# Performance work log

Hardware: AMD Instinct MI355X
Metric: run time of the kernel (lower is better)

## Reference

```python
import jax, jax.numpy as jnp
import numpy as np

L, B, Q, P, D, H, F = 3, 256, 128, 16, 256, 16, 512
DK = D // H
SCALE = DK ** -0.5  # lsa=False -> constant scale
EPS = 1e-5


def _ln(x, g, b):
    m = jnp.mean(x, axis=-1, keepdims=True)
    v = jnp.mean(jnp.square(x - m), axis=-1, keepdims=True)
    return (x - m) * jax.lax.rsqrt(v + EPS) * g + b


def setup_inputs() -> dict:
    key = jax.random.key(0)
    ks = jax.random.split(key, 12)
    w = lambda k, shape: 0.02 * jax.random.normal(k, shape, dtype=jnp.float32)
    return {
        "x": jax.random.normal(ks[0], (B, Q, P), dtype=jnp.float32),
        "attn_bias": 0.1 * jax.random.normal(ks[1], (1, Q, Q), dtype=jnp.float32),
        "W_P": w(ks[2], (P, D)), "b_P": jnp.zeros((D,), jnp.float32),
        "W_pos": w(ks[3], (Q, D)),
        "Wq": w(ks[4], (L, D, D)), "bq": jnp.zeros((L, D), jnp.float32),
        "Wk": w(ks[5], (L, D, D)), "bk": jnp.zeros((L, D), jnp.float32),
        "Wv": w(ks[6], (L, D, D)), "bv": jnp.zeros((L, D), jnp.float32),
        "Wo": w(ks[7], (L, D, D)), "bo": jnp.zeros((L, D), jnp.float32),
        "ln1_g": jnp.ones((L, D), jnp.float32), "ln1_b": jnp.zeros((L, D), jnp.float32),
        "W1": w(ks[8], (L, D, F)), "b1": jnp.zeros((L, F), jnp.float32),
        "W2": w(ks[9], (L, F, D)), "b2": jnp.zeros((L, D), jnp.float32),
        "ln2_g": jnp.ones((L, D), jnp.float32), "ln2_b": jnp.zeros((L, D), jnp.float32),
    }


def _encoder(x, attn_bias, W_P, b_P, W_pos,
             Wq, bq, Wk, bk, Wv, bv, Wo, bo, ln1_g, ln1_b,
             W1, b1, W2, b2, ln2_g, ln2_b):
    # patch embedding + positional encoding (dropout=0, eval mode)
    z = x @ W_P + b_P + W_pos                      # [B, Q, D]
    bias = attn_bias[:, None]                      # [1, 1, Q, Q]

    def layer(carry, p):
        z, prev = carry
        (wq, bq_, wk, bk_, wv, bv_, wo, bo_, g1, be1, w1, b1_, w2, b2_, g2, be2) = p
        q = (z @ wq + bq_).reshape(B, Q, H, DK).transpose(0, 2, 1, 3)  # [B,H,Q,dk]
        k = (z @ wk + bk_).reshape(B, Q, H, DK).transpose(0, 2, 1, 3)
        v = (z @ wv + bv_).reshape(B, Q, H, DK).transpose(0, 2, 1, 3)
        # residual-attention + bias-augmented scores
        scores = jnp.einsum('bhqd,bhkd->bhqk', q, k) * SCALE + prev + bias
        attn = jax.nn.softmax(scores, axis=-1)
        o = jnp.einsum('bhqk,bhkd->bhqd', attn, v)
        o = o.transpose(0, 2, 1, 3).reshape(B, Q, D) @ wo + bo_
        z = _ln(z + o, g1, be1)                     # post-norm
        ffo = jax.nn.gelu(z @ w1 + b1_, approximate=False) @ w2 + b2_
        z = _ln(z + ffo, g2, be2)
        return (z, scores), None

    prev0 = jnp.zeros((B, H, Q, Q), z.dtype)        # prev=None == add zero
    params = (Wq, bq, Wk, bk, Wv, bv, Wo, bo, ln1_g, ln1_b,
              W1, b1, W2, b2, ln2_g, ln2_b)
    (z, _), _ = jax.lax.scan(layer, (z, prev0), params)
    return z


def reference(x, attn_bias, W_P, b_P, W_pos, Wq, bq, Wk, bk, Wv, bv, Wo, bo,
              ln1_g, ln1_b, W1, b1, W2, b2, ln2_g, ln2_b):
    return _encoder(x, attn_bias, W_P, b_P, W_pos, Wq, bq, Wk, bk, Wv, bv,
                    Wo, bo, ln1_g, ln1_b, W1, b1, W2, b2, ln2_g, ln2_b)
```

## Files before the change

### kernel.cpp

```cpp
#include <hip/hip_runtime.h>

#define DEV __device__ __forceinline__

typedef float          f32x4  __attribute__((ext_vector_type(4)));
typedef __bf16         bf16x8 __attribute__((ext_vector_type(8)));
typedef unsigned short u16x8  __attribute__((ext_vector_type(8)));

static constexpr int  Bq   = 256;
static constexpr int  Qs   = 128;
static constexpr int  Dm   = 256;
static constexpr int  Ff   = 512;
static constexpr int  ROWS = Bq * Qs;
static constexpr long QK_LSTR = (long)ROWS * 512;

DEV float b2f(unsigned short h) {
    unsigned int u = ((unsigned int)h) << 16;
    float f; __builtin_memcpy(&f, &u, 4); return f;
}
DEV unsigned short f2b(float f) {
    unsigned int u; __builtin_memcpy(&u, &f, 4);
    u += 0x7fffu + ((u >> 16) & 1u);
    return (unsigned short)(u >> 16);
}
DEV f32x4 mfma_bf16(u16x8 a, u16x8 b, f32x4 c) {
    return __builtin_amdgcn_mfma_f32_16x16x32_bf16(
        __builtin_bit_cast(bf16x8, a), __builtin_bit_cast(bf16x8, b), c, 0, 0, 0);
}
DEV void gl_lds16(const unsigned short* g, unsigned short* l) {
    __builtin_amdgcn_global_load_lds(
        (const __attribute__((address_space(1))) unsigned int*)g,
        (__attribute__((address_space(3))) unsigned int*)l, 16, 0, 0);
}
DEV int zadr(int row, int col) {
    return row * 256 + ((((col >> 3) ^ (row & 7))) << 3) + (col & 7);
}

__global__ void k_embed(const float* __restrict__ x,
                        const float* __restrict__ WP,
                        const float* __restrict__ bP,
                        const float* __restrict__ Wpos,
                        unsigned short* __restrict__ zb) {
    int row = blockIdx.x;
    int d   = threadIdx.x;
    int q   = row & (Qs - 1);
    const float* xr = x + row * 16;
    float acc = bP[d] + Wpos[q * Dm + d];
#pragma unroll
    for (int p = 0; p < 16; p++) acc += xr[p] * WP[p * Dm + d];
    zb[(long)row * Dm + d] = f2b(acc);
}

static constexpr int S0 = 3 * 768 * 256;
static constexpr int S1 = 3 * 256 * 256;
static constexpr int S2 = 3 * 512 * 256;
static constexpr int S3 = 3 * 256 * 512;
static constexpr int S4 = 3 * 768;
static constexpr int S5 = 3 * 64 * 256;
static constexpr int PREP_TOT = S0 + S1 + S2 + S3 + S4 + S5;

__global__ void k_prep(const float* __restrict__ Wq, const float* __restrict__ Wk,
                       const float* __restrict__ Wv, const float* __restrict__ Wo,
                       const float* __restrict__ W1, const float* __restrict__ W2,
                       const float* __restrict__ bq, const float* __restrict__ bk,
                       const float* __restrict__ bv, const float* __restrict__ ab,
                       unsigned short* __restrict__ wTqkv, unsigned short* __restrict__ wTo,
                       unsigned short* __restrict__ wp1, unsigned short* __restrict__ wp2,
                       float* __restrict__ bqkv, float* __restrict__ pb) {
    int idx = blockIdx.x * 256 + threadIdx.x;
    if (idx < S0) {
        int l = idx / (768 * 256), r = idx % (768 * 256);
        int n = r / 256, k = r % 256;
        const float* W = (n < 256) ? Wq : (n < 512) ? Wk : Wv;
        float v = W[(long)l * 65536 + k * 256 + (n & 255)];
        if (n < 256) v *= 0.25f;
        wTqkv[idx] = f2b(v);
    } else if (idx < S0 + S1) {
        int j = idx - S0;
        int l = j / 65536, r = j % 65536, n = r / 256, k = r % 256;
        wTo[j] = f2b(Wo[(long)l * 65536 + k * 256 + n]);
    } else if (idx < S0 + S1 + S2) {
        int j = idx - S0 - S1;
        int l = j / 131072, r = j % 131072;
        int tile = r >> 9, le = r & 511, lane = le >> 3, e = le & 7;
        int ntile = tile >> 3, kk = tile & 7;
        int n = ntile * 16 + (lane & 15), k = kk * 32 + (lane >> 4) * 8 + e;
        wp1[j] = f2b(W1[(long)l * 131072 + k * 512 + n]);
    } else if (idx < S0 + S1 + S2 + S3) {
        int j = idx - S0 - S1 - S2;
        int l = j / 131072, r = j % 131072;
        int tile = r >> 9, le = r & 511, lane = le >> 3, e = le & 7;
        int ntile = tile >> 4, kk = tile & 15;
        int n = ntile * 16 + (lane & 15), k = kk * 32 + (lane >> 4) * 8 + e;
        wp2[j] = f2b(W2[(long)l * 131072 + k * 256 + n]);
    } else if (idx < S0 + S1 + S2 + S3 + S4) {
        int j = idx - S0 - S1 - S2 - S3;
        int l = j / 768, c = j % 768;
        float v = (c < 256) ? bq[l * 256 + c] * 0.25f
                : (c < 512) ? bk[l * 256 + c - 256]
                            : bv[l * 256 + c - 512];
        bqkv[j] = v;
    } else if (idx < PREP_TOT) {
        int j = idx - S0 - S1 - S2 - S3 - S4;
        int l = j / 16384, r = j % 16384;
        int u = r / 256, t = r % 256;
        int i = u >> 5, rr = (u >> 3) & 3, jj = u & 7;
        int wave = t >> 6, quad = (t >> 4) & 3, l16 = t & 15;
        int m = 32 * wave + 16 * i + 4 * quad + rr;
        int col = 16 * jj + l16;
        pb[j] = (float)(l + 1) * ab[m * 128 + col];
    }
}

template <int GELU, int MODE>
__global__ __launch_bounds__(256) void k_gemm(const unsigned short* __restrict__ A,
                                              const unsigned short* __restrict__ WT,
                                              const float* __restrict__ bias,
                                              unsigned short* __restrict__ outB,
                                              unsigned short* __restrict__ aux,
                                              int M, int N, int K) {
    __shared__ unsigned short smem[16384];
    unsigned short* As = smem;
    unsigned short* Bs = smem + 8192;
    const int tid  = threadIdx.x;
    const int wave = tid >> 6, lane = tid & 63, quad = lane >> 4, l16 = lane & 15;
    const int mq = wave >> 1, nq = wave & 1;
    const int m_blk = blockIdx.x * 128, n_blk = blockIdx.y * 128;
    const int c0 = tid, c1 = tid + 256;
    const int ra0 = c0 >> 2, ca0 = (c0 & 3) * 8;
    const int ra1 = c1 >> 2, ca1 = (c1 & 3) * 8;

    f32x4 acc[4][4] = {};

    for (int k0 = 0; k0 < K; k0 += 64) {
#pragma unroll
        for (int hh = 0; hh < 2; hh++) {
            int kk = k0 + hh * 32;
            gl_lds16(A  + (long)(m_blk + ra0) * K + kk + ca0, &As[hh * 4096 + c0 * 8]);
            gl_lds16(A  + (long)(m_blk + ra1) * K + kk + ca1, &As[hh * 4096 + c1 * 8]);
            gl_lds16(WT + (long)(n_blk + ra0) * K + kk + ca0, &Bs[hh * 4096 + c0 * 8]);
            gl_lds16(WT + (long)(n_blk + ra1) * K + kk + ca1, &Bs[hh * 4096 + c1 * 8]);
        }
        __syncthreads();
#pragma unroll
        for (int hh = 0; hh < 2; hh++) {
            u16x8 af[4], bf[4];
#pragma unroll
            for (int i = 0; i < 4; i++)
                af[i] = *(const u16x8*)&As[hh * 4096 + (64 * mq + 16 * i + l16) * 32 + quad * 8];
#pragma unroll
            for (int j = 0; j < 4; j++)
                bf[j] = *(const u16x8*)&Bs[hh * 4096 + (64 * nq + 16 * j + l16) * 32 + quad * 8];
#pragma unroll
            for (int i = 0; i < 4; i++)
#pragma unroll
                for (int j = 0; j < 4; j++)
                    acc[i][j] = mfma_bf16(af[i], bf[j], acc[i][j]);
        }
        __syncthreads();
    }

#pragma unroll
    for (int i = 0; i < 4; i++) {
        int rl = 64 * mq + 16 * i + quad * 4;
#pragma unroll
        for (int j = 0; j < 4; j++) {
            int cl = 64 * nq + 16 * j + l16;
            float bb = bias[n_blk + cl];
#pragma unroll
            for (int r = 0; r < 4; r++) {
                float v = acc[i][j][r] + bb;
                if (GELU) v = 0.5f * v * (1.0f + erff(v * 0.70710678118f));
                if (MODE == 0) smem[(rl + r) * 128 + cl] = f2b(v);
                if (MODE == 2) {
                    int g = 4 * nq + j;
                    smem[g * 2048 + (rl + r) * 16 + l16] = f2b(v);
                }
            }
        }
    }
    __syncthreads();
#pragma unroll
    for (int c = tid; c < 2048; c += 256) {
        u16x8 val = *(const u16x8*)&smem[c * 8];
        if (MODE == 0) {
            int row = c >> 4, seg = c & 15;
            *(u16x8*)&outB[(long)(m_blk + row) * N + n_blk + seg * 8] = val;
        }
        if (MODE == 2) {
            int g = c >> 8, w = c & 255;
            int n = n_blk + g * 16;
            if (n < 512) {
                int s = n >> 8, h = (n >> 4) & 15;
                *(u16x8*)&outB[((long)(((m_blk >> 7) * 16 + h) * 2 + s)) * 2048 + w * 8] = val;
            } else {
                int hh = (n - 512) >> 4;
                *(u16x8*)&aux[((long)hh * ROWS + m_blk) * 16 + w * 8] = val;
            }
        }
    }
}

template <int LAST, int AHM>
__global__ __launch_bounds__(256) void k_gemm_ln(const unsigned short* __restrict__ A,
                                                 const unsigned short* __restrict__ WT,
                                                 const float* __restrict__ bias,
                                                 const unsigned short* __restrict__ Zres,
                                                 const float* __restrict__ g,
                                                 const float* __restrict__ be,
                                                 unsigned short* __restrict__ zb,
                                                 float* __restrict__ outF,
                                                 int K) {
    __shared__ unsigned short smem[16384 + 2048 + 8192];
    unsigned short* Zs = smem;
    unsigned short* As = smem + 16384;
    unsigned short* Bs = smem + 16384 + 2048;
    float2* stats = (float2*)(smem + 16384);

    const int tid  = threadIdx.x;
    const int wave = tid >> 6, lane = tid & 63, quad = lane >> 4, l16 = lane & 15;
    const int m_blk = blockIdx.x * 64;

#pragma unroll
    for (int s = 0; s < 8; s++) {
        int c = tid + 256 * s;
        int zr = c >> 5, zc = (c & 31) * 8;
        gl_lds16(Zres + (long)(m_blk + zr) * 256 + zc, &Zs[c * 8]);
    }

    const int ca = (tid & 3) * 8, raA = tid >> 2;
    f32x4 acc[4][4] = {};

    for (int k0 = 0; k0 < K; k0 += 32) {
        if (AHM) {
            int k = k0 + ca;
            gl_lds16(A + ((long)(k >> 4) * ROWS + m_blk + raA) * 16 + (k & 15), &As[tid * 8]);
        } else {
            gl_lds16(A + (long)(m_blk + raA) * K + k0 + ca, &As[tid * 8]);
        }
#pragma unroll
        for (int s = 0; s < 4; s++) {
            int c = tid + 256 * s;
            int br = c >> 2, bc = (c & 3) * 8;
            gl_lds16(WT + (long)br * K + k0 + bc, &Bs[c * 8]);
        }
        __syncthreads();
        u16x8 af[4], bf[4];
#pragma unroll
        for (int i = 0; i < 4; i++)
            af[i] = *(const u16x8*)&As[(16 * i + l16) * 32 + quad * 8];
#pragma unroll
        for (int j = 0; j < 4; j++)
            bf[j] = *(const u16x8*)&Bs[(64 * wave + 16 * j + l16) * 32 + quad * 8];
#pragma unroll
        for (int i = 0; i < 4; i++)
#pragma unroll
            for (int j = 0; j < 4; j++)
                acc[i][j] = mfma_bf16(af[i], bf[j], acc[i][j]);
        __syncthreads();
    }

    float bb[4], gg[4], bt[4];
#pragma unroll
    for (int j = 0; j < 4; j++) {
        int col = 64 * wave + 16 * j + l16;
        bb[j] = bias[col]; gg[j] = g[col]; bt[j] = be[col];
    }
#pragma unroll
    for (int i = 0; i < 4; i++) {
#pragma unroll
        for (int r = 0; r < 4; r++) {
            int rloc = 16 * i + quad * 4 + r;
            float s1 = 0.f, s2 = 0.f;
#pragma unroll
            for (int j = 0; j < 4; j++) {
                int col = 64 * wave + 16 * j + l16;
                float v = acc[i][j][r] + bb[j] + b2f(Zs[rloc * 256 + col]);
                acc[i][j][r] = v;
                s1 += v; s2 += v * v;
            }
            for (int mk = 1; mk < 16; mk <<= 1) {
                s1 += __shfl_xor(s1, mk);
                s2 += __shfl_xor(s2, mk);
            }
            if (l16 == 0) stats[rloc * 4 + wave] = make_float2(s1, s2);
        }
    }
    __syncthreads();
#pragma unroll
    for (int i = 0; i < 4; i++) {
#pragma unroll
        for (int r = 0; r < 4; r++) {
            int rloc = 16 * i + quad * 4 + r;
            f32x4 p0 = *(const f32x4*)&stats[rloc * 4];
            f32x4 p1 = *(const f32x4*)&stats[rloc * 4 + 2];
            float S1 = p0[0] + p0[2] + p1[0] + p1[2];
            float S2 = p0[1] + p0[3] + p1[1] + p1[3];
            float mean = S1 * (1.0f / 256.0f);
            float var  = S2 * (1.0f / 256.0f) - mean * mean;
            float rstd = rsqrtf(var + 1e-5f);
            long grow = m_blk + rloc;
#pragma unroll
            for (int j = 0; j < 4; j++) {
                int col = 64 * wave + 16 * j + l16;
                float o = (acc[i][j][r] - mean) * rstd * gg[j] + bt[j];
                if (LAST) outF[grow * 256 + col] = o;
                else      zb[grow * 256 + col] = f2b(o);
            }
        }
    }
}

template <int LAST>
__global__ __launch_bounds__(256, 2) void k_ffn(const unsigned short* __restrict__ zin,
                                                const unsigned short* __restrict__ wp1,
                                                const float* __restrict__ b1,
                                                const unsigned short* __restrict__ wp2,
                                                const float* __restrict__ b2,
                                                const float* __restrict__ g2,
                                                const float* __restrict__ be2,
                                                unsigned short* __restrict__ zout,
                                                float* __restrict__ outF) {
    __shared__ unsigned short Zs[64 * 256];
    __shared__ unsigned short Hs[64 * 256];
    __shared__ float2 stats[64 * 4];

    const int tid  = threadIdx.x;
    const int wave = tid >> 6, lane = tid & 63, quad = (lane >> 4) & 3, l16 = lane & 15;
    const int m_blk = blockIdx.x * 64;

    {
        int row = tid >> 2;
#pragma unroll
        for (int cc = 0; cc < 8; cc++) {
            int c0 = (tid & 3) * 64 + cc * 8;
            u16x8 v = *(const u16x8*)&zin[(long)(m_blk + row) * 256 + c0];
            *(u16x8*)&Zs[zadr(row, c0)] = v;
        }
    }
    __syncthreads();

    f32x4 z2[4][4] = {};
#pragma unroll 1
    for (int c = 0; c < 2; c++) {
        f32x4 a1[4][4] = {};
#pragma unroll 2
        for (int kk = 0; kk < 8; kk++) {
            u16x8 af[4], bf[4];
#pragma unroll
            for (int i = 0; i < 4; i++)
                af[i] = *(const u16x8*)&Zs[(16 * i + l16) * 256 + (((kk * 4 + quad) ^ (l16 & 7)) << 3)];
#pragma unroll
            for (int j = 0; j < 4; j++)
                bf[j] = *(const u16x8*)&wp1[((long)(16 * c + 4 * wave + j) * 8 + kk) * 512 + lane * 8];
#pragma unroll
            for (int i = 0; i < 4; i++)
#pragma unroll
                for (int j = 0; j < 4; j++)
                    a1[i][j] = mfma_bf16(af[i], bf[j], a1[i][j]);
        }
        __syncthreads();
        float b1v[4];
#pragma unroll
        for (int j = 0; j < 4; j++) b1v[j] = b1[256 * c + 64 * wave + 16 * j + l16];
#pragma unroll
        for (int i = 0; i < 4; i++)
#pragma unroll
            for (int j = 0; j < 4; j++)
#pragma unroll
                for (int r = 0; r < 4; r++) {
                    int row  = 16 * i + quad * 4 + r;
                    int colh = 64 * wave + 16 * j + l16;
                    float v = a1[i][j][r] + b1v[j];
                    float gel = 0.5f * v * (1.0f + erff(v * 0.70710678118f));
                    Hs[zadr(row, colh)] = f2b(gel);
                }
        __syncthreads();
#pragma unroll 2
        for (int kk = 0; kk < 8; kk++) {
            u16x8 af[4], bf[4];
#pragma unroll
            for (int i = 0; i < 4; i++)
                af[i] = *(const u16x8*)&Hs[(16 * i + l16) * 256 + (((kk * 4 + quad) ^ (l16 & 7)) << 3)];
#pragma unroll
            for (int j = 0; j < 4; j++)
                bf[j] = *(const u16x8*)&wp2[((long)(4 * wave + j) * 16 + 8 * c + kk) * 512 + lane * 8];
#pragma unroll
            for (int i = 0; i < 4; i++)
#pragma unroll
                for (int j = 0; j < 4; j++)
                    z2[i][j] = mfma_bf16(af[i], bf[j], z2[i][j]);
        }
    }

    float b2v[4], gg[4], bb[4];
#pragma unroll
    for (int j = 0; j < 4; j++) {
        int col = 64 * wave + 16 * j + l16;
        b2v[j] = b2[col]; gg[j] = g2[col]; bb[j] = be2[col];
    }
#pragma unroll
    for (int i = 0; i < 4; i++)
#pragma unroll
        for (int r = 0; r < 4; r++) {
            int row = 16 * i + quad * 4 + r;
            float s1 = 0.f, s2 = 0.f;
#pragma unroll
            for (int j = 0; j < 4; j++) {
                int col = 64 * wave + 16 * j + l16;
                float v = z2[i][j][r] + b2v[j] + b2f(Zs[zadr(row, col)]);
                z2[i][j][r] = v; s1 += v; s2 += v * v;
            }
            for (int mk = 1; mk < 16; mk <<= 1) { s1 += __shfl_xor(s1, mk); s2 += __shfl_xor(s2, mk); }
            if (l16 == 0) stats[row * 4 + wave] = make_float2(s1, s2);
        }
    __syncthreads();
#pragma unroll
    for (int i = 0; i < 4; i++)
#pragma unroll
        for (int r = 0; r < 4; r++) {
            int row = 16 * i + quad * 4 + r;
            f32x4 p0 = *(const f32x4*)&stats[row * 4];
            f32x4 p1 = *(const f32x4*)&stats[row * 4 + 2];
            float S1 = p0[0] + p0[2] + p1[0] + p1[2];
            float S2 = p0[1] + p0[3] + p1[1] + p1[3];
            float mean = S1 * (1.0f / 256.0f);
            float var  = S2 * (1.0f / 256.0f) - mean * mean;
            float rstd = rsqrtf(var + 1e-5f);
            long grow = m_blk + row;
#pragma unroll
            for (int j = 0; j < 4; j++) {
                int col = 64 * wave + 16 * j + l16;
                float o = (z2[i][j][r] - mean) * rstd * gg[j] + bb[j];
                if (LAST) outF[grow * 256 + col] = o;
                else      zout[grow * 256 + col] = f2b(o);
            }
        }
}

template <int L>
__global__ __launch_bounds__(256) void k_attn(const unsigned short* __restrict__ qkh,
                                              const unsigned short* __restrict__ vbuf,
                                              const float* __restrict__ pb,
                                              unsigned short* __restrict__ o_out) {
    __shared__ unsigned short vt[16 * 136];
    __shared__ unsigned short Ps[128 * 136];
    const int tid  = threadIdx.x;
    const int wave = tid >> 6, lane = tid & 63, quad = lane >> 4, l16 = lane & 15;
    const int b = blockIdx.x >> 4, h = blockIdx.x & 15;
    const int qrow = tid >> 1, half = tid & 1;

    u16x8 vv = *(const u16x8*)(vbuf + ((long)h * ROWS + b * Qs + qrow) * 16 + half * 8);
    const float* pbt = pb + (long)L * 16384 + tid;

    f32x4 accS[2][8] = {};
    u16x8 zero = {};

    constexpr int FULL = (L + 1) / 2;
    constexpr bool HALF = ((L + 1) & 1) != 0;

#pragma unroll
    for (int p = 0; p < FULL; p++) {
        const unsigned short* q0 = qkh + ((long)(((2 * p) * Bq + b) * 16 + h) * 2) * 2048;
        const unsigned short* q1 = qkh + ((long)(((2 * p + 1) * Bq + b) * 16 + h) * 2) * 2048;
        const unsigned short* qsel = (quad < 2) ? q0 : q1;
        const unsigned short* ksel = (quad < 2) ? (q0 + 2048) : (q1 + 2048);
        const int koff = (quad & 1) * 8;
        u16x8 af[2], bf8[8];
#pragma unroll
        for (int i = 0; i < 2; i++) {
            int m = 32 * wave + 16 * i + l16;
            af[i] = *(const u16x8*)(qsel + m * 16 + koff);
        }
#pragma unroll
        for (int j = 0; j < 8; j++) {
            int n = 16 * j + l16;
            bf8[j] = *(const u16x8*)(ksel + n * 16 + koff);
        }
#pragma unroll
        for (int i = 0; i < 2; i++)
#pragma unroll
            for (int j = 0; j < 8; j++)
                accS[i][j] = mfma_bf16(af[i], bf8[j], accS[i][j]);
    }
    if (HALF) {
        const unsigned short* qt = qkh + ((long)((L * Bq + b) * 16 + h) * 2) * 2048;
        const unsigned short* kt = qt + 2048;
        u16x8 af[2], bf8[8];
#pragma unroll
        for (int i = 0; i < 2; i++) {
            int m = 32 * wave + 16 * i + l16;
            af[i] = (quad < 2) ? *(const u16x8*)(qt + m * 16 + quad * 8) : zero;
        }
#pragma unroll
        for (int j = 0; j < 8; j++) {
            int n = 16 * j + l16;
            bf8[j] = (quad < 2) ? *(const u16x8*)(kt + n * 16 + quad * 8) : zero;
        }
#pragma unroll
        for (int i = 0; i < 2; i++)
#pragma unroll
            for (int j = 0; j < 8; j++)
                accS[i][j] = mfma_bf16(af[i], bf8[j], accS[i][j]);
    }

#pragma unroll
    for (int jj = 0; jj < 8; jj++) vt[(half * 8 + jj) * 136 + qrow] = vv[jj];

#pragma unroll
    for (int i = 0; i < 2; i++) {
#pragma unroll
        for (int r = 0; r < 4; r++) {
            int m = 32 * wave + 16 * i + quad * 4 + r;
#pragma unroll
            for (int j = 0; j < 8; j++) {
                int u = (i * 4 + r) * 8 + j;
                float s = accS[i][j][r] + pbt[u * 256];
                Ps[m * 136 + 16 * j + l16] = f2b(__expf(s));
            }
        }
    }
    __syncthreads();

    f32x4 accO[2] = {};
    f32x4 accR[2] = {};
    u16x8 ones;
#pragma unroll
    for (int jj = 0; jj < 8; jj++) ones[jj] = 0x3F80;
#pragma unroll
    for (int s = 0; s < 4; s++) {
        u16x8 bv = *(const u16x8*)&vt[l16 * 136 + s * 32 + quad * 8];
#pragma unroll
        for (int i = 0; i < 2; i++) {
            u16x8 ap = *(const u16x8*)&Ps[(32 * wave + 16 * i + l16) * 136 + s * 32 + quad * 8];
            accO[i] = mfma_bf16(ap, bv, accO[i]);
            accR[i] = mfma_bf16(ap, ones, accR[i]);
        }
    }
    __syncthreads();
#pragma unroll
    for (int i = 0; i < 2; i++)
#pragma unroll
        for (int r = 0; r < 4; r++) {
            int m = 32 * wave + 16 * i + quad * 4 + r;
            float inv = __builtin_amdgcn_rcpf(accR[i][r]);
            vt[m * 16 + l16] = f2b(accO[i][r] * inv);
        }
    __syncthreads();
    {
        unsigned short* obase = o_out + ((long)h * ROWS + b * Qs) * 16;
        *(u16x8*)&obase[tid * 8] = *(const u16x8*)&vt[tid * 8];
    }
}

extern "C" void kernel_launch(void* const* d_in, const int* in_sizes, int n_in,
                              void* d_out, int out_size, void* d_ws, size_t ws_size,
                              hipStream_t stream) {
    const float* x     = (const float*)d_in[0];
    const float* abias = (const float*)d_in[1];
    const float* WP    = (const float*)d_in[2];
    const float* bP    = (const float*)d_in[3];
    const float* Wpos  = (const float*)d_in[4];
    const float* Wq    = (const float*)d_in[5];
    const float* bqp   = (const float*)d_in[6];
    const float* Wk    = (const float*)d_in[7];
    const float* bkp   = (const float*)d_in[8];
    const float* Wv    = (const float*)d_in[9];
    const float* bvp   = (const float*)d_in[10];
    const float* Wo    = (const float*)d_in[11];
    const float* bo    = (const float*)d_in[12];
    const float* g1    = (const float*)d_in[13];
    const float* be1   = (const float*)d_in[14];
    const float* W1    = (const float*)d_in[15];
    const float* b1    = (const float*)d_in[16];
    const float* W2    = (const float*)d_in[17];
    const float* b2    = (const float*)d_in[18];
    const float* g2    = (const float*)d_in[19];
    const float* be2   = (const float*)d_in[20];
    (void)in_sizes; (void)n_in; (void)out_size; (void)ws_size;

    char* ws = (char*)d_ws;
    size_t off = 0;
    auto alloc = [&](size_t bytes) -> char* {
        char* p = ws + off; off += (bytes + 255) & ~(size_t)255; return p;
    };
    unsigned short* z_b   = (unsigned short*)alloc((size_t)ROWS * Dm * 2);
    unsigned short* qkh   = (unsigned short*)alloc((size_t)3 * ROWS * 512 * 2);
    unsigned short* v_cur = (unsigned short*)alloc((size_t)ROWS * Dm * 2);
    unsigned short* o_b   = (unsigned short*)alloc((size_t)ROWS * Dm * 2);
    unsigned short* wTqkv = (unsigned short*)alloc((size_t)S0 * 2);
    unsigned short* wTo   = (unsigned short*)alloc((size_t)S1 * 2);
    unsigned short* wp1   = (unsigned short*)alloc((size_t)S2 * 2);
    unsigned short* wp2   = (unsigned short*)alloc((size_t)S3 * 2);
    float*          bqkv  = (float*)alloc((size_t)S4 * 4);
    float*          pb    = (float*)alloc((size_t)S5 * 4);

    k_prep<<<(PREP_TOT + 255) / 256, 256, 0, stream>>>(
        Wq, Wk, Wv, Wo, W1, W2, bqp, bkp, bvp, abias,
        wTqkv, wTo, wp1, wp2, bqkv, pb);
    k_embed<<<ROWS, 256, 0, stream>>>(x, WP, bP, Wpos, z_b);

    for (int l = 0; l < 3; l++) {
        k_gemm<0, 2><<<dim3(ROWS / 128, 6), 256, 0, stream>>>(
            z_b, wTqkv + (long)l * 768 * 256, bqkv + l * 768,
            qkh + (long)l * QK_LSTR, v_cur, ROWS, 768, 256);
        if (l == 0)      k_attn<0><<<Bq * 16, 256, 0, stream>>>(qkh, v_cur, pb, o_b);
        else if (l == 1) k_attn<1><<<Bq * 16, 256, 0, stream>>>(qkh, v_cur, pb, o_b);
        else             k_attn<2><<<Bq * 16, 256, 0, stream>>>(qkh, v_cur, pb, o_b);
        k_gemm_ln<0, 1><<<ROWS / 64, 256, 0, stream>>>(
            o_b, wTo + (long)l * 256 * 256, bo + l * 256, z_b,
            g1 + l * 256, be1 + l * 256, z_b, nullptr, 256);
        if (l == 2)
            k_ffn<1><<<ROWS / 64, 256, 0, stream>>>(
                z_b, wp1 + (long)l * 131072, b1 + l * 512,
                wp2 + (long)l * 131072, b2 + l * 256,
                g2 + l * 256, be2 + l * 256, nullptr, (float*)d_out);
        else
            k_ffn<0><<<ROWS / 64, 256, 0, stream>>>(
                z_b, wp1 + (long)l * 131072, b1 + l * 512,
                wp2 + (long)l * 131072, b2 + l * 256,
                g2 + l * 256, be2 + l * 256, z_b, nullptr);
    }
}
```

Before: 500.3 us.

## Fuse output projection and first LayerNorm into the FFN kernel

Removes the separate k_gemm_ln launch by computing the attention output projection, residual add and LayerNorm inside k_ffn, keeping the normalized rows in LDS for the FFN instead of writing z to global memory and reading it back. Wo is prepacked into the MFMA fragment layout so B fragments load straight from global memory. The FFN k-loops also double-buffer their weight fragment loads. This saves one launch and a full activation round trip per layer, at the cost of extra register pressure in an already heavy fused kernel.

```diff
diff --git a/kernel.cpp b/kernel.cpp
--- a/kernel.cpp
+++ b/kernel.cpp
@@ -63,7 +63,7 @@
                        const float* __restrict__ W1, const float* __restrict__ W2,
                        const float* __restrict__ bq, const float* __restrict__ bk,
                        const float* __restrict__ bv, const float* __restrict__ ab,
-                       unsigned short* __restrict__ wTqkv, unsigned short* __restrict__ wTo,
+                       unsigned short* __restrict__ wTqkv, unsigned short* __restrict__ wpO,
                        unsigned short* __restrict__ wp1, unsigned short* __restrict__ wp2,
                        float* __restrict__ bqkv, float* __restrict__ pb) {
     int idx = blockIdx.x * 256 + threadIdx.x;
@@ -76,8 +76,11 @@
         wTqkv[idx] = f2b(v);
     } else if (idx < S0 + S1) {
         int j = idx - S0;
-        int l = j / 65536, r = j % 65536, n = r / 256, k = r % 256;
-        wTo[j] = f2b(Wo[(long)l * 65536 + k * 256 + n]);
+        int l = j / 65536, r = j % 65536;
+        int tile = r >> 9, le = r & 511, lane = le >> 3, e = le & 7;
+        int ntile = tile >> 3, kk = tile & 7;
+        int n = ntile * 16 + (lane & 15), k = kk * 32 + (lane >> 4) * 8 + e;
+        wpO[j] = f2b(Wo[(long)l * 65536 + k * 256 + n]);
     } else if (idx < S0 + S1 + S2) {
         int j = idx - S0 - S1;
         int l = j / 131072, r = j % 131072;
@@ -200,142 +203,102 @@
     }
 }
 
-template <int LAST, int AHM>
-__global__ __launch_bounds__(256) void k_gemm_ln(const unsigned short* __restrict__ A,
-                                                 const unsigned short* __restrict__ WT,
-                                                 const float* __restrict__ bias,
-                                                 const unsigned short* __restrict__ Zres,
-                                                 const float* __restrict__ g,
-                                                 const float* __restrict__ be,
-                                                 unsigned short* __restrict__ zb,
-                                                 float* __restrict__ outF,
-                                                 int K) {
-    __shared__ unsigned short smem[16384 + 2048 + 8192];
-    unsigned short* Zs = smem;
-    unsigned short* As = smem + 16384;
-    unsigned short* Bs = smem + 16384 + 2048;
-    float2* stats = (float2*)(smem + 16384);
+template <int LAST>
+__global__ __launch_bounds__(256, 2) void k_ffn(
+    const unsigned short* __restrict__ zin,
+    const unsigned short* __restrict__ ob,
+    const unsigned short* __restrict__ wpO, const float* __restrict__ bo,
+    const float* __restrict__ g1, const float* __restrict__ be1,
+    const unsigned short* __restrict__ wp1, const float* __restrict__ b1,
+    const unsigned short* __restrict__ wp2, const float* __restrict__ b2,
+    const float* __restrict__ g2, const float* __restrict__ be2,
+    unsigned short* __restrict__ zout, float* __restrict__ outF) {
+    __shared__ unsigned short Zs[64 * 256];
+    __shared__ unsigned short Hs[64 * 256];
+    float2* stats = (float2*)Hs;
 
     const int tid  = threadIdx.x;
-    const int wave = tid >> 6, lane = tid & 63, quad = lane >> 4, l16 = lane & 15;
+    const int wave = tid >> 6, lane = tid & 63, quad = (lane >> 4) & 3, l16 = lane & 15;
     const int m_blk = blockIdx.x * 64;
 
 #pragma unroll
     for (int s = 0; s < 8; s++) {
         int c = tid + 256 * s;
         int zr = c >> 5, zc = (c & 31) * 8;
-        gl_lds16(Zres + (long)(m_blk + zr) * 256 + zc, &Zs[c * 8]);
-    }
-
-    const int ca = (tid & 3) * 8, raA = tid >> 2;
-    f32x4 acc[4][4] = {};
-
-    for (int k0 = 0; k0 < K; k0 += 32) {
-        if (AHM) {
-            int k = k0 + ca;
-            gl_lds16(A + ((long)(k >> 4) * ROWS + m_blk + raA) * 16 + (k & 15), &As[tid * 8]);
-        } else {
-            gl_lds16(A + (long)(m_blk + raA) * K + k0 + ca, &As[tid * 8]);
-        }
-#pragma unroll
-        for (int s = 0; s < 4; s++) {
-            int c = tid + 256 * s;
-            int br = c >> 2, bc = (c & 3) * 8;
-            gl_lds16(WT + (long)br * K + k0 + bc, &Bs[c * 8]);
-        }
+        u16x8 vz = *(const u16x8*)&zin[(long)(m_blk + zr) * 256 + zc];
+        *(u16x8*)&Zs[zadr(zr, zc)] = vz;
+        int h = c >> 7, rem = c & 127, orow = rem >> 1, half = rem & 1;
+        u16x8 vo = *(const u16x8*)&ob[((long)h * ROWS + m_blk + orow) * 16 + half * 8];
+        *(u16x8*)&Hs[zadr(orow, h * 16 + half * 8)] = vo;
+    }
+    __syncthreads();
+
+    f32x4 accO[4][4] = {};
+    {
+        u16x8 bf[2][4];
+#pragma unroll
+        for (int j = 0; j < 4; j++)
+            bf[0][j] = *(const u16x8*)&wpO[((long)(4 * wave + j) * 8 + 0) * 512 + lane * 8];
+#pragma unroll
+        for (int kk = 0; kk < 8; kk++) {
+            if (kk < 7)
+#pragma unroll
+                for (int j = 0; j < 4; j++)
+                    bf[(kk + 1) & 1][j] = *(const u16x8*)&wpO[((long)(4 * wave + j) * 8 + kk + 1) * 512 + lane * 8];
+            u16x8 af[4];
+#pragma unroll
+            for (int i = 0; i < 4; i++)
+                af[i] = *(const u16x8*)&Hs[(16 * i + l16) * 256 + (((kk * 4 + quad) ^ (l16 & 7)) << 3)];
+#pragma unroll
+            for (int i = 0; i < 4; i++)
+#pragma unroll
+                for (int j = 0; j < 4; j++)
+                    accO[i][j] = mfma_bf16(af[i], bf[kk & 1][j], accO[i][j]);
+        }
+    }
+    __syncthreads();
+
+    {
+        float bb[4], gg[4], bt[4];
+#pragma unroll
+        for (int j = 0; j < 4; j++) {
+            int col = 64 * wave + 16 * j + l16;
+            bb[j] = bo[col]; gg[j] = g1[col]; bt[j] = be1[col];
+        }
+#pragma unroll
+        for (int i = 0; i < 4; i++)
+#pragma unroll
+            for (int r = 0; r < 4; r++) {
+                int row = 16 * i + quad * 4 + r;
+                float s1 = 0.f, s2 = 0.f;
+#pragma unroll
+                for (int j = 0; j < 4; j++) {
+                    int col = 64 * wave + 16 * j + l16;
+                    float v = accO[i][j][r] + bb[j] + b2f(Zs[zadr(row, col)]);
+                    accO[i][j][r] = v; s1 += v; s2 += v * v;
+                }
+                for (int mk = 1; mk < 16; mk <<= 1) { s1 += __shfl_xor(s1, mk); s2 += __shfl_xor(s2, mk); }
+                if (l16 == 0) stats[row * 4 + wave] = make_float2(s1, s2);
+            }
         __syncthreads();
-        u16x8 af[4], bf[4];
 #pragma unroll
         for (int i = 0; i < 4; i++)
-            af[i] = *(const u16x8*)&As[(16 * i + l16) * 32 + quad * 8];
-#pragma unroll
-        for (int j = 0; j < 4; j++)
-            bf[j] = *(const u16x8*)&Bs[(64 * wave + 16 * j + l16) * 32 + quad * 8];
-#pragma unroll
-        for (int i = 0; i < 4; i++)
-#pragma unroll
-            for (int j = 0; j < 4; j++)
-                acc[i][j] = mfma_bf16(af[i], bf[j], acc[i][j]);
-        __syncthreads();
-    }
-
-    float bb[4], gg[4], bt[4];
-#pragma unroll
-    for (int j = 0; j < 4; j++) {
-        int col = 64 * wave + 16 * j + l16;
-        bb[j] = bias[col]; gg[j] = g[col]; bt[j] = be[col];
-    }
-#pragma unroll
-    for (int i = 0; i < 4; i++) {
-#pragma unroll
-        for (int r = 0; r < 4; r++) {
-            int rloc = 16 * i + quad * 4 + r;
-            float s1 = 0.f, s2 = 0.f;
-#pragma unroll
-            for (int j = 0; j < 4; j++) {
-                int col = 64 * wave + 16 * j + l16;
-                float v = acc[i][j][r] + bb[j] + b2f(Zs[rloc * 256 + col]);
-                acc[i][j][r] = v;
-                s1 += v; s2 += v * v;
-            }
-            for (int mk = 1; mk < 16; mk <<= 1) {
-                s1 += __shfl_xor(s1, mk);
-                s2 += __shfl_xor(s2, mk);
-            }
-            if (l16 == 0) stats[rloc * 4 + wave] = make_float2(s1, s2);
-        }
-    }
-    __syncthreads();
-#pragma unroll
-    for (int i = 0; i < 4; i++) {
-#pragma unroll
-        for (int r = 0; r < 4; r++) {
-            int rloc = 16 * i + quad * 4 + r;
-            f32x4 p0 = *(const f32x4*)&stats[rloc * 4];
-            f32x4 p1 = *(const f32x4*)&stats[rloc * 4 + 2];
-            float S1 = p0[0] + p0[2] + p1[0] + p1[2];
-            float S2 = p0[1] + p0[3] + p1[1] + p1[3];
-            float mean = S1 * (1.0f / 256.0f);
-            float var  = S2 * (1.0f / 256.0f) - mean * mean;
-            float rstd = rsqrtf(var + 1e-5f);
-            long grow = m_blk + rloc;
-#pragma unroll
-            for (int j = 0; j < 4; j++) {
-                int col = 64 * wave + 16 * j + l16;
-                float o = (acc[i][j][r] - mean) * rstd * gg[j] + bt[j];
-                if (LAST) outF[grow * 256 + col] = o;
-                else      zb[grow * 256 + col] = f2b(o);
-            }
-        }
-    }
-}
-
-template <int LAST>
-__global__ __launch_bounds__(256, 2) void k_ffn(const unsigned short* __restrict__ zin,
-                                                const unsigned short* __restrict__ wp1,
-                                                const float* __restrict__ b1,
-                                                const unsigned short* __restrict__ wp2,
-                                                const float* __restrict__ b2,
-                                                const float* __restrict__ g2,
-                                                const float* __restrict__ be2,
-                                                unsigned short* __restrict__ zout,
-                                                float* __restrict__ outF) {
-    __shared__ unsigned short Zs[64 * 256];
-    __shared__ unsigned short Hs[64 * 256];
-    __shared__ float2 stats[64 * 4];
-
-    const int tid  = threadIdx.x;
-    const int wave = tid >> 6, lane = tid & 63, quad = (lane >> 4) & 3, l16 = lane & 15;
-    const int m_blk = blockIdx.x * 64;
-
-    {
-        int row = tid >> 2;
-#pragma unroll
-        for (int cc = 0; cc < 8; cc++) {
-            int c0 = (tid & 3) * 64 + cc * 8;
-            u16x8 v = *(const u16x8*)&zin[(long)(m_blk + row) * 256 + c0];
-            *(u16x8*)&Zs[zadr(row, c0)] = v;
-        }
+#pragma unroll
+            for (int r = 0; r < 4; r++) {
+                int row = 16 * i + quad * 4 + r;
+                f32x4 p0 = *(const f32x4*)&stats[row * 4];
+                f32x4 p1 = *(const f32x4*)&stats[row * 4 + 2];
+                float S1 = p0[0] + p0[2] + p1[0] + p1[2];
+                float S2 = p0[1] + p0[3] + p1[1] + p1[3];
+                float mean = S1 * (1.0f / 256.0f);
+                float var  = S2 * (1.0f / 256.0f) - mean * mean;
+                float rstd = rsqrtf(var + 1e-5f);
+#pragma unroll
+                for (int j = 0; j < 4; j++) {
+                    int col = 64 * wave + 16 * j + l16;
+                    Zs[zadr(row, col)] = f2b((accO[i][j][r] - mean) * rstd * gg[j] + bt[j]);
+                }
+            }
     }
     __syncthreads();
 
@@ -343,20 +306,27 @@
 #pragma unroll 1
     for (int c = 0; c < 2; c++) {
         f32x4 a1[4][4] = {};
-#pragma unroll 2
-        for (int kk = 0; kk < 8; kk++) {
-            u16x8 af[4], bf[4];
-#pragma unroll
-            for (int i = 0; i < 4; i++)
-                af[i] = *(const u16x8*)&Zs[(16 * i + l16) * 256 + (((kk * 4 + quad) ^ (l16 & 7)) << 3)];
+        {
+            u16x8 bf[2][4];
 #pragma unroll
             for (int j = 0; j < 4; j++)
-                bf[j] = *(const u16x8*)&wp1[((long)(16 * c + 4 * wave + j) * 8 + kk) * 512 + lane * 8];
-#pragma unroll
-            for (int i = 0; i < 4; i++)
-#pragma unroll
-                for (int j = 0; j < 4; j++)
-                    a1[i][j] = mfma_bf16(af[i], bf[j], a1[i][j]);
+                bf[0][j] = *(const u16x8*)&wp1[((long)(16 * c + 4 * wave + j) * 8 + 0) * 512 + lane * 8];
+#pragma unroll
+            for (int kk = 0; kk < 8; kk++) {
+                if (kk < 7)
+#pragma unroll
+                    for (int j = 0; j < 4; j++)
+                        bf[(kk + 1) & 1][j] = *(const u16x8*)&wp1[((long)(16 * c + 4 * wave + j) * 8 + kk + 1) * 512 + lane * 8];
+                u16x8 af[4];
+#pragma unroll
+                for (int i = 0; i < 4; i++)
+                    af[i] = *(const u16x8*)&Zs[(16 * i + l16) * 256 + (((kk * 4 + quad) ^ (l16 & 7)) << 3)];
+#pragma unroll
+                for (int i = 0; i < 4; i++)
+#pragma unroll
+                    for (int j = 0; j < 4; j++)
+                        a1[i][j] = mfma_bf16(af[i], bf[kk & 1][j], a1[i][j]);
+            }
         }
         __syncthreads();
         float b1v[4];
@@ -375,22 +345,30 @@
                     Hs[zadr(row, colh)] = f2b(gel);
                 }
         __syncthreads();
-#pragma unroll 2
-        for (int kk = 0; kk < 8; kk++) {
-            u16x8 af[4], bf[4];
-#pragma unroll
-            for (int i = 0; i < 4; i++)
-                af[i] = *(const u16x8*)&Hs[(16 * i + l16) * 256 + (((kk * 4 + quad) ^ (l16 & 7)) << 3)];
+        {
+            u16x8 bg[2][4];
 #pragma unroll
             for (int j = 0; j < 4; j++)
-                bf[j] = *(const u16x8*)&wp2[((long)(4 * wave + j) * 16 + 8 * c + kk) * 512 + lane * 8];
-#pragma unroll
-            for (int i = 0; i < 4; i++)
-#pragma unroll
-                for (int j = 0; j < 4; j++)
-                    z2[i][j] = mfma_bf16(af[i], bf[j], z2[i][j]);
-        }
-    }
+                bg[0][j] = *(const u16x8*)&wp2[((long)(4 * wave + j) * 16 + 8 * c + 0) * 512 + lane * 8];
+#pragma unroll
+            for (int kk = 0; kk < 8; kk++) {
+                if (kk < 7)
+#pragma unroll
+                    for (int j = 0; j < 4; j++)
+                        bg[(kk + 1) & 1][j] = *(const u16x8*)&wp2[((long)(4 * wave + j) * 16 + 8 * c + kk + 1) * 512 + lane * 8];
+                u16x8 af[4];
+#pragma unroll
+                for (int i = 0; i < 4; i++)
+                    af[i] = *(const u16x8*)&Hs[(16 * i + l16) * 256 + (((kk * 4 + quad) ^ (l16 & 7)) << 3)];
+#pragma unroll
+                for (int i = 0; i < 4; i++)
+#pragma unroll
+                    for (int j = 0; j < 4; j++)
+                        z2[i][j] = mfma_bf16(af[i], bg[kk & 1][j], z2[i][j]);
+            }
+        }
+    }
+    __syncthreads();
 
     float b2v[4], gg[4], bb[4];
 #pragma unroll
@@ -588,7 +566,7 @@
     unsigned short* v_cur = (unsigned short*)alloc((size_t)ROWS * Dm * 2);
     unsigned short* o_b   = (unsigned short*)alloc((size_t)ROWS * Dm * 2);
     unsigned short* wTqkv = (unsigned short*)alloc((size_t)S0 * 2);
-    unsigned short* wTo   = (unsigned short*)alloc((size_t)S1 * 2);
+    unsigned short* wpO   = (unsigned short*)alloc((size_t)S1 * 2);
     unsigned short* wp1   = (unsigned short*)alloc((size_t)S2 * 2);
     unsigned short* wp2   = (unsigned short*)alloc((size_t)S3 * 2);
     float*          bqkv  = (float*)alloc((size_t)S4 * 4);
@@ -596,7 +574,7 @@
 
     k_prep<<<(PREP_TOT + 255) / 256, 256, 0, stream>>>(
         Wq, Wk, Wv, Wo, W1, W2, bqp, bkp, bvp, abias,
-        wTqkv, wTo, wp1, wp2, bqkv, pb);
+        wTqkv, wpO, wp1, wp2, bqkv, pb);
     k_embed<<<ROWS, 256, 0, stream>>>(x, WP, bP, Wpos, z_b);
 
     for (int l = 0; l < 3; l++) {
@@ -606,18 +584,19 @@
         if (l == 0)      k_attn<0><<<Bq * 16, 256, 0, stream>>>(qkh, v_cur, pb, o_b);
         else if (l == 1) k_attn<1><<<Bq * 16, 256, 0, stream>>>(qkh, v_cur, pb, o_b);
         else             k_attn<2><<<Bq * 16, 256, 0, stream>>>(qkh, v_cur, pb, o_b);
-        k_gemm_ln<0, 1><<<ROWS / 64, 256, 0, stream>>>(
-            o_b, wTo + (long)l * 256 * 256, bo + l * 256, z_b,
-            g1 + l * 256, be1 + l * 256, z_b, nullptr, 256);
-        if (l == 2)
+        if (l < 2)
+            k_ffn<0><<<ROWS / 64, 256, 0, stream>>>(
+                z_b, o_b, wpO + (long)l * 65536, bo + l * 256,
+                g1 + l * 256, be1 + l * 256,
+                wp1 + (long)l * 131072, b1 + l * 512,
+                wp2 + (long)l * 131072, b2 + l * 256,
+                g2 + l * 256, be2 + l * 256, z_b, nullptr);
+        else
             k_ffn<1><<<ROWS / 64, 256, 0, stream>>>(
-                z_b, wp1 + (long)l * 131072, b1 + l * 512,
+                z_b, o_b, wpO + (long)l * 65536, bo + l * 256,
+                g1 + l * 256, be1 + l * 256,
+                wp1 + (long)l * 131072, b1 + l * 512,
                 wp2 + (long)l * 131072, b2 + l * 256,
                 g2 + l * 256, be2 + l * 256, nullptr, (float*)d_out);
-        else
-            k_ffn<0><<<ROWS / 64, 256, 0, stream>>>(
-                z_b, wp1 + (long)l * 131072, b1 + l * 512,
-                wp2 + (long)l * 131072, b2 + l * 256,
-                g2 + l * 256, be2 + l * 256, z_b, nullptr);
-    }
-}
+    }
+}
```

Measured after the change: 706.8 us. 41.3% more time.

## Fuse next layer's QKV projection into FFN epilogue with smaller row tiles

Applied to the files above, without the earlier changes.

The FFN kernel now keeps the normalized output rows in shared memory and immediately computes the next layer's Q/K/V projection from them, writing straight into the attention-ready buffers. This removes the separate QKV GEMM launch and one reread of z for layers 1 and 2. The FFN tile shrinks from 64 to 32 rows, occupancy rises to 4 blocks per SM, and B-operand loads are double-buffered in registers. A new pre-packed QKV weight layout is added in the prep kernel. The cost is extra per-block weight traffic, since each 32-row block now rereads the full QKV and FFN weights.

```diff
diff --git a/kernel.cpp b/kernel.cpp
--- a/kernel.cpp
+++ b/kernel.cpp
@@ -50,57 +50,70 @@
     zb[(long)row * Dm + d] = f2b(acc);
 }
 
-static constexpr int S0 = 3 * 768 * 256;
-static constexpr int S1 = 3 * 256 * 256;
-static constexpr int S2 = 3 * 512 * 256;
-static constexpr int S3 = 3 * 256 * 512;
-static constexpr int S4 = 3 * 768;
-static constexpr int S5 = 3 * 64 * 256;
-static constexpr int PREP_TOT = S0 + S1 + S2 + S3 + S4 + S5;
+static constexpr int S0a = 3 * 768 * 256;
+static constexpr int S0b = 3 * 768 * 256;
+static constexpr int S1  = 3 * 256 * 256;
+static constexpr int S2  = 3 * 512 * 256;
+static constexpr int S3  = 3 * 256 * 512;
+static constexpr int S4  = 3 * 768;
+static constexpr int S5  = 3 * 64 * 256;
+static constexpr int PREP_TOT = S0a + S0b + S1 + S2 + S3 + S4 + S5;
 
 __global__ void k_prep(const float* __restrict__ Wq, const float* __restrict__ Wk,
                        const float* __restrict__ Wv, const float* __restrict__ Wo,
                        const float* __restrict__ W1, const float* __restrict__ W2,
                        const float* __restrict__ bq, const float* __restrict__ bk,
                        const float* __restrict__ bv, const float* __restrict__ ab,
-                       unsigned short* __restrict__ wTqkv, unsigned short* __restrict__ wTo,
+                       unsigned short* __restrict__ wTqkv, unsigned short* __restrict__ wpQ,
+                       unsigned short* __restrict__ wTo,
                        unsigned short* __restrict__ wp1, unsigned short* __restrict__ wp2,
                        float* __restrict__ bqkv, float* __restrict__ pb) {
     int idx = blockIdx.x * 256 + threadIdx.x;
-    if (idx < S0) {
+    if (idx < S0a) {
         int l = idx / (768 * 256), r = idx % (768 * 256);
         int n = r / 256, k = r % 256;
         const float* W = (n < 256) ? Wq : (n < 512) ? Wk : Wv;
         float v = W[(long)l * 65536 + k * 256 + (n & 255)];
         if (n < 256) v *= 0.25f;
         wTqkv[idx] = f2b(v);
-    } else if (idx < S0 + S1) {
-        int j = idx - S0;
+    } else if (idx < S0a + S0b) {
+        int j = idx - S0a;
+        int l = j / 196608, r = j % 196608;
+        int tile = r >> 9, le = r & 511, lane = le >> 3, e = le & 7;
+        int ntile = tile >> 3, kk = tile & 7;
+        int n = ntile * 16 + (lane & 15), k = kk * 32 + (lane >> 4) * 8 + e;
+        float v;
+        if (n < 256)      v = Wq[(long)l * 65536 + k * 256 + n] * 0.25f;
+        else if (n < 512) v = Wk[(long)l * 65536 + k * 256 + (n - 256)];
+        else              v = Wv[(long)l * 65536 + k * 256 + (n - 512)];
+        wpQ[j] = f2b(v);
+    } else if (idx < S0a + S0b + S1) {
+        int j = idx - S0a - S0b;
         int l = j / 65536, r = j % 65536, n = r / 256, k = r % 256;
         wTo[j] = f2b(Wo[(long)l * 65536 + k * 256 + n]);
-    } else if (idx < S0 + S1 + S2) {
-        int j = idx - S0 - S1;
+    } else if (idx < S0a + S0b + S1 + S2) {
+        int j = idx - S0a - S0b - S1;
         int l = j / 131072, r = j % 131072;
         int tile = r >> 9, le = r & 511, lane = le >> 3, e = le & 7;
         int ntile = tile >> 3, kk = tile & 7;
         int n = ntile * 16 + (lane & 15), k = kk * 32 + (lane >> 4) * 8 + e;
         wp1[j] = f2b(W1[(long)l * 131072 + k * 512 + n]);
-    } else if (idx < S0 + S1 + S2 + S3) {
-        int j = idx - S0 - S1 - S2;
+    } else if (idx < S0a + S0b + S1 + S2 + S3) {
+        int j = idx - S0a - S0b - S1 - S2;
         int l = j / 131072, r = j % 131072;
         int tile = r >> 9, le = r & 511, lane = le >> 3, e = le & 7;
         int ntile = tile >> 4, kk = tile & 15;
         int n = ntile * 16 + (lane & 15), k = kk * 32 + (lane >> 4) * 8 + e;
         wp2[j] = f2b(W2[(long)l * 131072 + k * 256 + n]);
-    } else if (idx < S0 + S1 + S2 + S3 + S4) {
-        int j = idx - S0 - S1 - S2 - S3;
+    } else if (idx < S0a + S0b + S1 + S2 + S3 + S4) {
+        int j = idx - S0a - S0b - S1 - S2 - S3;
         int l = j / 768, c = j % 768;
         float v = (c < 256) ? bq[l * 256 + c] * 0.25f
                 : (c < 512) ? bk[l * 256 + c - 256]
                             : bv[l * 256 + c - 512];
         bqkv[j] = v;
     } else if (idx < PREP_TOT) {
-        int j = idx - S0 - S1 - S2 - S3 - S4;
+        int j = idx - S0a - S0b - S1 - S2 - S3 - S4;
         int l = j / 16384, r = j % 16384;
         int u = r / 256, t = r % 256;
         int i = u >> 5, rr = (u >> 3) & 3, jj = u & 7;
@@ -311,59 +324,63 @@
 }
 
 template <int LAST>
-__global__ __launch_bounds__(256, 2) void k_ffn(const unsigned short* __restrict__ zin,
-                                                const unsigned short* __restrict__ wp1,
-                                                const float* __restrict__ b1,
-                                                const unsigned short* __restrict__ wp2,
-                                                const float* __restrict__ b2,
-                                                const float* __restrict__ g2,
-                                                const float* __restrict__ be2,
-                                                unsigned short* __restrict__ zout,
-                                                float* __restrict__ outF) {
-    __shared__ unsigned short Zs[64 * 256];
-    __shared__ unsigned short Hs[64 * 256];
-    __shared__ float2 stats[64 * 4];
+__global__ __launch_bounds__(256, 4) void k_ffn(
+    const unsigned short* __restrict__ zin,
+    const unsigned short* __restrict__ wp1, const float* __restrict__ b1,
+    const unsigned short* __restrict__ wp2, const float* __restrict__ b2,
+    const float* __restrict__ g2, const float* __restrict__ be2,
+    unsigned short* __restrict__ zout, float* __restrict__ outF,
+    const unsigned short* __restrict__ wpQ, const float* __restrict__ bqn,
+    unsigned short* __restrict__ qkhn, unsigned short* __restrict__ vcurn) {
+    __shared__ unsigned short Zs[32 * 256];
+    __shared__ unsigned short Hs[32 * 256];
+    float2* stats = (float2*)Hs;
 
     const int tid  = threadIdx.x;
     const int wave = tid >> 6, lane = tid & 63, quad = (lane >> 4) & 3, l16 = lane & 15;
-    const int m_blk = blockIdx.x * 64;
-
-    {
-        int row = tid >> 2;
-#pragma unroll
-        for (int cc = 0; cc < 8; cc++) {
-            int c0 = (tid & 3) * 64 + cc * 8;
-            u16x8 v = *(const u16x8*)&zin[(long)(m_blk + row) * 256 + c0];
-            *(u16x8*)&Zs[zadr(row, c0)] = v;
-        }
+    const int m_blk = blockIdx.x * 32;
+
+#pragma unroll
+    for (int s = 0; s < 4; s++) {
+        int c = tid + 256 * s;
+        int zr = c >> 5, zc = (c & 31) * 8;
+        u16x8 v = *(const u16x8*)&zin[(long)(m_blk + zr) * 256 + zc];
+        *(u16x8*)&Zs[zadr(zr, zc)] = v;
     }
     __syncthreads();
 
-    f32x4 z2[4][4] = {};
+    f32x4 z2[2][4] = {};
 #pragma unroll 1
     for (int c = 0; c < 2; c++) {
-        f32x4 a1[4][4] = {};
-#pragma unroll 2
-        for (int kk = 0; kk < 8; kk++) {
-            u16x8 af[4], bf[4];
-#pragma unroll
-            for (int i = 0; i < 4; i++)
-                af[i] = *(const u16x8*)&Zs[(16 * i + l16) * 256 + (((kk * 4 + quad) ^ (l16 & 7)) << 3)];
+        f32x4 a1[2][4] = {};
+        {
+            u16x8 bf[2][4];
 #pragma unroll
             for (int j = 0; j < 4; j++)
-                bf[j] = *(const u16x8*)&wp1[((long)(16 * c + 4 * wave + j) * 8 + kk) * 512 + lane * 8];
-#pragma unroll
-            for (int i = 0; i < 4; i++)
-#pragma unroll
-                for (int j = 0; j < 4; j++)
-                    a1[i][j] = mfma_bf16(af[i], bf[j], a1[i][j]);
+                bf[0][j] = *(const u16x8*)&wp1[((long)(16 * c + 4 * wave + j) * 8 + 0) * 512 + lane * 8];
+#pragma unroll
+            for (int kk = 0; kk < 8; kk++) {
+                if (kk < 7)
+#pragma unroll
+                    for (int j = 0; j < 4; j++)
+                        bf[(kk + 1) & 1][j] = *(const u16x8*)&wp1[((long)(16 * c + 4 * wave + j) * 8 + kk + 1) * 512 + lane * 8];
+                u16x8 af[2];
+#pragma unroll
+                for (int i = 0; i < 2; i++)
+                    af[i] = *(const u16x8*)&Zs[(16 * i + l16) * 256 + (((kk * 4 + quad) ^ (l16 & 7)) << 3)];
+#pragma unroll
+                for (int i = 0; i < 2; i++)
+#pragma unroll
+                    for (int j = 0; j < 4; j++)
+                        a1[i][j] = mfma_bf16(af[i], bf[kk & 1][j], a1[i][j]);
+            }
         }
         __syncthreads();
         float b1v[4];
 #pragma unroll
         for (int j = 0; j < 4; j++) b1v[j] = b1[256 * c + 64 * wave + 16 * j + l16];
 #pragma unroll
-        for (int i = 0; i < 4; i++)
+        for (int i = 0; i < 2; i++)
 #pragma unroll
             for (int j = 0; j < 4; j++)
 #pragma unroll
@@ -375,22 +392,30 @@
                     Hs[zadr(row, colh)] = f2b(gel);
                 }
         __syncthreads();
-#pragma unroll 2
-        for (int kk = 0; kk < 8; kk++) {
-            u16x8 af[4], bf[4];
-#pragma unroll
-            for (int i = 0; i < 4; i++)
-                af[i] = *(const u16x8*)&Hs[(16 * i + l16) * 256 + (((kk * 4 + quad) ^ (l16 & 7)) << 3)];
+        {
+            u16x8 bg[2][4];
 #pragma unroll
             for (int j = 0; j < 4; j++)
-                bf[j] = *(const u16x8*)&wp2[((long)(4 * wave + j) * 16 + 8 * c + kk) * 512 + lane * 8];
-#pragma unroll
-            for (int i = 0; i < 4; i++)
-#pragma unroll
-                for (int j = 0; j < 4; j++)
-                    z2[i][j] = mfma_bf16(af[i], bf[j], z2[i][j]);
-        }
-    }
+                bg[0][j] = *(const u16x8*)&wp2[((long)(4 * wave + j) * 16 + 8 * c + 0) * 512 + lane * 8];
+#pragma unroll
+            for (int kk = 0; kk < 8; kk++) {
+                if (kk < 7)
+#pragma unroll
+                    for (int j = 0; j < 4; j++)
+                        bg[(kk + 1) & 1][j] = *(const u16x8*)&wp2[((long)(4 * wave + j) * 16 + 8 * c + kk + 1) * 512 + lane * 8];
+                u16x8 af[2];
+#pragma unroll
+                for (int i = 0; i < 2; i++)
+                    af[i] = *(const u16x8*)&Hs[(16 * i + l16) * 256 + (((kk * 4 + quad) ^ (l16 & 7)) << 3)];
+#pragma unroll
+                for (int i = 0; i < 2; i++)
+#pragma unroll
+                    for (int j = 0; j < 4; j++)
+                        z2[i][j] = mfma_bf16(af[i], bg[kk & 1][j], z2[i][j]);
+            }
+        }
+    }
+    __syncthreads();
 
     float b2v[4], gg[4], bb[4];
 #pragma unroll
@@ -399,7 +424,7 @@
         b2v[j] = b2[col]; gg[j] = g2[col]; bb[j] = be2[col];
     }
 #pragma unroll
-    for (int i = 0; i < 4; i++)
+    for (int i = 0; i < 2; i++)
 #pragma unroll
         for (int r = 0; r < 4; r++) {
             int row = 16 * i + quad * 4 + r;
@@ -415,7 +440,7 @@
         }
     __syncthreads();
 #pragma unroll
-    for (int i = 0; i < 4; i++)
+    for (int i = 0; i < 2; i++)
 #pragma unroll
         for (int r = 0; r < 4; r++) {
             int row = 16 * i + quad * 4 + r;
@@ -431,10 +456,71 @@
             for (int j = 0; j < 4; j++) {
                 int col = 64 * wave + 16 * j + l16;
                 float o = (z2[i][j][r] - mean) * rstd * gg[j] + bb[j];
-                if (LAST) outF[grow * 256 + col] = o;
-                else      zout[grow * 256 + col] = f2b(o);
-            }
-        }
+                if constexpr (LAST) {
+                    outF[grow * 256 + col] = o;
+                } else {
+                    unsigned short hv = f2b(o);
+                    Zs[zadr(row, col)] = hv;
+                    zout[grow * 256 + col] = hv;
+                }
+            }
+        }
+
+    if constexpr (!LAST) {
+        __syncthreads();
+        const int bb_ = m_blk >> 7;
+        const int rbase = m_blk & 127;
+#pragma unroll 1
+        for (int p = 0; p < 3; p++) {
+            f32x4 aq[2][4] = {};
+            {
+                u16x8 bf[2][4];
+#pragma unroll
+                for (int j = 0; j < 4; j++)
+                    bf[0][j] = *(const u16x8*)&wpQ[((long)(16 * p + 4 * wave + j) * 8 + 0) * 512 + lane * 8];
+#pragma unroll
+                for (int kk = 0; kk < 8; kk++) {
+                    if (kk < 7)
+#pragma unroll
+                        for (int j = 0; j < 4; j++)
+                            bf[(kk + 1) & 1][j] = *(const u16x8*)&wpQ[((long)(16 * p + 4 * wave + j) * 8 + kk + 1) * 512 + lane * 8];
+                    u16x8 af[2];
+#pragma unroll
+                    for (int i = 0; i < 2; i++)
+                        af[i] = *(const u16x8*)&Zs[(16 * i + l16) * 256 + (((kk * 4 + quad) ^ (l16 & 7)) << 3)];
+#pragma unroll
+                    for (int i = 0; i < 2; i++)
+#pragma unroll
+                        for (int j = 0; j < 4; j++)
+                            aq[i][j] = mfma_bf16(af[i], bf[kk & 1][j], aq[i][j]);
+                }
+            }
+#pragma unroll
+            for (int j = 0; j < 4; j++) {
+                int col = 256 * p + 64 * wave + 16 * j + l16;
+                float bqv = bqn[col];
+                int h = 4 * wave + j;
+                if (p < 2) {
+                    unsigned short* qk = qkhn + ((long)((bb_ * 16 + h) * 2 + p)) * 2048;
+#pragma unroll
+                    for (int i = 0; i < 2; i++)
+#pragma unroll
+                        for (int r = 0; r < 4; r++) {
+                            int rin = rbase + 16 * i + quad * 4 + r;
+                            qk[rin * 16 + l16] = f2b(aq[i][j][r] + bqv);
+                        }
+                } else {
+#pragma unroll
+                    for (int i = 0; i < 2; i++)
+#pragma unroll
+                        for (int r = 0; r < 4; r++) {
+                            long grow = m_blk + 16 * i + quad * 4 + r;
+                            vcurn[((long)h * ROWS + grow) * 16 + l16] = f2b(aq[i][j][r] + bqv);
+                        }
+                }
+            }
+        }
+    }
 }
 
 template <int L>
@@ -587,7 +673,8 @@
     unsigned short* qkh   = (unsigned short*)alloc((size_t)3 * ROWS * 512 * 2);
     unsigned short* v_cur = (unsigned short*)alloc((size_t)ROWS * Dm * 2);
     unsigned short* o_b   = (unsigned short*)alloc((size_t)ROWS * Dm * 2);
-    unsigned short* wTqkv = (unsigned short*)alloc((size_t)S0 * 2);
+    unsigned short* wTqkv = (unsigned short*)alloc((size_t)S0a * 2);
+    unsigned short* wpQ   = (unsigned short*)alloc((size_t)S0b * 2);
     unsigned short* wTo   = (unsigned short*)alloc((size_t)S1 * 2);
     unsigned short* wp1   = (unsigned short*)alloc((size_t)S2 * 2);
     unsigned short* wp2   = (unsigned short*)alloc((size_t)S3 * 2);
@@ -596,28 +683,31 @@
 
     k_prep<<<(PREP_TOT + 255) / 256, 256, 0, stream>>>(
         Wq, Wk, Wv, Wo, W1, W2, bqp, bkp, bvp, abias,
-        wTqkv, wTo, wp1, wp2, bqkv, pb);
+        wTqkv, wpQ, wTo, wp1, wp2, bqkv, pb);
     k_embed<<<ROWS, 256, 0, stream>>>(x, WP, bP, Wpos, z_b);
 
+    k_gemm<0, 2><<<dim3(ROWS / 128, 6), 256, 0, stream>>>(
+        z_b, wTqkv, bqkv, qkh, v_cur, ROWS, 768, 256);
+
     for (int l = 0; l < 3; l++) {
-        k_gemm<0, 2><<<dim3(ROWS / 128, 6), 256, 0, stream>>>(
-            z_b, wTqkv + (long)l * 768 * 256, bqkv + l * 768,
-            qkh + (long)l * QK_LSTR, v_cur, ROWS, 768, 256);
         if (l == 0)      k_attn<0><<<Bq * 16, 256, 0, stream>>>(qkh, v_cur, pb, o_b);
         else if (l == 1) k_attn<1><<<Bq * 16, 256, 0, stream>>>(qkh, v_cur, pb, o_b);
         else             k_attn<2><<<Bq * 16, 256, 0, stream>>>(qkh, v_cur, pb, o_b);
         k_gemm_ln<0, 1><<<ROWS / 64, 256, 0, stream>>>(
             o_b, wTo + (long)l * 256 * 256, bo + l * 256, z_b,
             g1 + l * 256, be1 + l * 256, z_b, nullptr, 256);
-        if (l == 2)
-            k_ffn<1><<<ROWS / 64, 256, 0, stream>>>(
+        if (l < 2)
+            k_ffn<0><<<ROWS / 32, 256, 0, stream>>>(
                 z_b, wp1 + (long)l * 131072, b1 + l * 512,
                 wp2 + (long)l * 131072, b2 + l * 256,
-                g2 + l * 256, be2 + l * 256, nullptr, (float*)d_out);
+                g2 + l * 256, be2 + l * 256, z_b, nullptr,
+                wpQ + (long)(l + 1) * 196608, bqkv + (l + 1) * 768,
+                qkh + (long)(l + 1) * QK_LSTR, v_cur);
         else
-            k_ffn<0><<<ROWS / 64, 256, 0, stream>>>(
+            k_ffn<1><<<ROWS / 32, 256, 0, stream>>>(
                 z_b, wp1 + (long)l * 131072, b1 + l * 512,
                 wp2 + (long)l * 131072, b2 + l * 256,
-                g2 + l * 256, be2 + l * 256, z_b, nullptr);
-    }
-}
+                g2 + l * 256, be2 + l * 256, nullptr, (float*)d_out,
+                nullptr, nullptr, nullptr, nullptr);
+    }
+}
```

Result: slower. 685.4 us (+37.0%).
